# Kernel tuning notes

Measured on AMD Instinct MI355X. Metric: run time of the kernel, lower is better.

The kernel has to match this reference:

```python
import jax, jax.numpy as jnp
import numpy as np

BS, X_DIM, KEY_DIM, N_KEYS, TOPK = 16384, 4096, 512, 4096, 16


def setup_inputs() -> dict:
    key = jax.random.key(0)
    k_x, k_keys, k_w, k_b = jax.random.split(key, 4)
    bound = 1.0 / np.sqrt(X_DIM)  # torch Linear default init range
    return {
        "x": jax.random.normal(k_x, (BS, X_DIM), dtype=jnp.float32),
        "keys": jax.random.normal(k_keys, (N_KEYS, KEY_DIM), dtype=jnp.float32),
        "W": jax.random.uniform(k_w, (KEY_DIM, X_DIM), dtype=jnp.float32, minval=-bound, maxval=bound),
        "b": jax.random.uniform(k_b, (KEY_DIM,), dtype=jnp.float32, minval=-bound, maxval=bound),
        "topk": TOPK,
    }


def reference(x, keys, W, b, topk):
    # query = projection(x): [bs, key_dim]
    query = jnp.einsum("bx,kx->bk", x, W) + b
    # scores = query @ keys^T: [bs, n_keys]
    scores = jnp.einsum("bd,nd->bn", query, keys)
    real_topk = min(keys.shape[0], topk)
    topk_scores, topk_idx = jax.lax.top_k(scores, real_topk)  # [bs, k]
    bs = scores.shape[0]
    rows = jnp.arange(bs)[:, None]
    # scatter topk scores into a zero tensor, then softmax over the full row
    gates = jnp.zeros_like(scores).at[rows, topk_idx].set(topk_scores)
    gates = jax.nn.softmax(gates, axis=1)
    return (gates, scores)
```

## Files before the change

### kernel.cpp

```cpp
#include <hip/hip_runtime.h>
#include <stdint.h>

#define BS_T   16384
#define XDIM   4096
#define KDIM   512
#define NKEYS  4096
#define KTOP   16

typedef _Float16 half8  __attribute__((ext_vector_type(8)));
typedef _Float16 half4  __attribute__((ext_vector_type(4)));
typedef float    floatx4 __attribute__((ext_vector_type(4)));

__device__ static inline void gload_lds16(const void* g, void* l) {
  __builtin_amdgcn_global_load_lds(
      (const __attribute__((address_space(1))) uint32_t*)(uintptr_t)g,
      (__attribute__((address_space(3))) uint32_t*)(uint32_t)(uintptr_t)l,
      16, 0, 0);
}

#define SBAR() __builtin_amdgcn_sched_barrier(0)
#define FULL_BAR() do { __builtin_amdgcn_sched_barrier(0); \
                        __builtin_amdgcn_s_barrier(); \
                        __builtin_amdgcn_sched_barrier(0); } while (0)

__global__ __launch_bounds__(256) void cvt_f32_f16_v(const float* __restrict__ in,
                                                     _Float16* __restrict__ out, int n8) {
  int stride = gridDim.x * 256;
  for (int i = blockIdx.x * 256 + threadIdx.x; i < n8; i += stride) {
    float4 v0 = ((const float4*)in)[2 * i];
    float4 v1 = ((const float4*)in)[2 * i + 1];
    half8 h = { (_Float16)v0.x, (_Float16)v0.y, (_Float16)v0.z, (_Float16)v0.w,
                (_Float16)v1.x, (_Float16)v1.y, (_Float16)v1.z, (_Float16)v1.w };
    ((half8*)out)[i] = h;
  }
}

__global__ __launch_bounds__(512, 1)
void gemm1_pipe(const float* __restrict__ X, const _Float16* __restrict__ Wh,
                const float* __restrict__ bias, _Float16* __restrict__ Q) {
  __shared__ __align__(16) _Float16 ldsA[2][64 * 64];
  __shared__ __align__(16) _Float16 ldsB[2][512 * 64];

  const int tid  = threadIdx.x;
  const int lane = tid & 63;
  const int wid  = tid >> 6;
  const int rowBase = blockIdx.x * 64;
  const int rot  = (blockIdx.x * 29) & 63;
  const int wc  = wid * 64;
  const int l15 = lane & 15;
  const int q4  = lane >> 4;
  const int sub   = lane >> 3;
  const int gslot = (lane & 7) ^ sub;

  auto KT = [&](int t) { return ((t + rot) & 63) * 64; };

  const int r0 = tid >> 4,          s0 = tid & 15;
  const int r1 = (tid + 512) >> 4,  s1 = (tid + 512) & 15;
  const float* aSrc0 = X + (size_t)(rowBase + r0) * XDIM + s0 * 4;
  const float* aSrc1 = X + (size_t)(rowBase + r1) * XDIM + s1 * 4;
  const int aoff0 = r0 * 128 + (((s0 >> 1) * 16) ^ ((r0 & 7) << 4)) + (s0 & 1) * 8;
  const int aoff1 = r1 * 128 + (((s1 >> 1) * 16) ^ ((r1 & 7) << 4)) + (s1 & 1) * 8;

  const _Float16* const bSrc = Wh + (size_t)(wc + sub) * XDIM + gslot * 8;

  auto stageB = [&](int kt, int buf) {
    char* bd = (char*)&ldsB[buf][0] + wid * 8192;
    #pragma unroll
    for (int i = 0; i < 8; ++i)
      gload_lds16(bSrc + (size_t)i * 8 * XDIM + kt, bd + i * 1024);
  };
  auto writeA = [&](int buf, float4 v0, float4 v1) {
    half4 h0 = { (_Float16)v0.x, (_Float16)v0.y, (_Float16)v0.z, (_Float16)v0.w };
    half4 h1 = { (_Float16)v1.x, (_Float16)v1.y, (_Float16)v1.z, (_Float16)v1.w };
    *(half4*)((char*)&ldsA[buf][0] + aoff0) = h0;
    *(half4*)((char*)&ldsA[buf][0] + aoff1) = h1;
  };
  auto ld8 = [&](const char* base, int row, int s) {
    return *(const half8*)(base + row * 128 + ((s * 16) ^ ((row & 7) << 4)));
  };

  floatx4 acc[4][4];
  #pragma unroll
  for (int m = 0; m < 4; ++m)
    #pragma unroll
    for (int n = 0; n < 4; ++n)
      acc[m][n] = (floatx4)0.0f;

  float4 p0  = *(const float4*)(aSrc0 + KT(0));
  float4 p1  = *(const float4*)(aSrc1 + KT(0));
  float4 aw0 = *(const float4*)(aSrc0 + KT(1));
  float4 aw1 = *(const float4*)(aSrc1 + KT(1));
  stageB(KT(0), 0);
  stageB(KT(1), 1);
  writeA(0, p0, p1);
  asm volatile("s_waitcnt lgkmcnt(0)" ::: "memory");
  asm volatile("s_waitcnt vmcnt(8)" ::: "memory");
  FULL_BAR();

  #pragma unroll 2
  for (int t = 0; t < 64; ++t) {
    const int cu = t & 1;
    const char* bA = (const char*)&ldsA[cu][0];
    const char* bB = (const char*)&ldsB[cu][0];

    half8 a[4][2], b[4][2];
    #pragma unroll
    for (int m = 0; m < 4; ++m)
      #pragma unroll
      for (int kk = 0; kk < 2; ++kk)
        a[m][kk] = ld8(bA, m * 16 + l15, kk * 4 + q4);
    #pragma unroll
    for (int n = 0; n < 4; ++n)
      #pragma unroll
      for (int kk = 0; kk < 2; ++kk)
        b[n][kk] = ld8(bB, wc + n * 16 + l15, kk * 4 + q4);
    float4 nl0, nl1;
    if (t < 62) {
      nl0 = *(const float4*)(aSrc0 + KT(t + 2));
      nl1 = *(const float4*)(aSrc1 + KT(t + 2));
    }
    asm volatile("s_waitcnt lgkmcnt(0)" ::: "memory");
    __builtin_amdgcn_sched_barrier(0);
    if (t < 62) stageB(KT(t + 2), cu);
    __builtin_amdgcn_sched_barrier(0);

    __builtin_amdgcn_s_setprio(1);
    #pragma unroll
    for (int m = 0; m < 4; ++m)
      #pragma unroll
      for (int n = 0; n < 4; ++n)
        #pragma unroll
        for (int kk = 0; kk < 2; ++kk)
          acc[m][n] = __builtin_amdgcn_mfma_f32_16x16x32_f16(a[m][kk], b[n][kk], acc[m][n], 0, 0, 0);
    __builtin_amdgcn_s_setprio(0);

    if (t < 63) writeA(cu ^ 1, aw0, aw1);
    asm volatile("s_waitcnt lgkmcnt(0)" ::: "memory");
    __builtin_amdgcn_sched_barrier(0);
    if (t < 62)       asm volatile("s_waitcnt vmcnt(10)" ::: "memory");
    else if (t == 62) asm volatile("s_waitcnt vmcnt(0)"  ::: "memory");
    FULL_BAR();
    aw0 = nl0; aw1 = nl1;
  }

  #pragma unroll
  for (int m = 0; m < 4; ++m) {
    #pragma unroll
    for (int n = 0; n < 4; ++n) {
      int col = wc + n * 16 + l15;
      float bv = bias[col];
      #pragma unroll
      for (int r = 0; r < 4; ++r) {
        int row = rowBase + m * 16 + q4 * 4 + r;
        Q[(size_t)row * KDIM + col] = (_Float16)(acc[m][n][r] + bv);
      }
    }
  }
}

__global__ __launch_bounds__(512, 2)
void gemm2_pipe(const _Float16* __restrict__ Aq, const _Float16* __restrict__ Bk,
                float* __restrict__ outp) {
  __shared__ __align__(16) _Float16 ldsA[2][256 * 64];
  __shared__ __align__(16) _Float16 ldsB[2][256 * 64];

  const int tid  = threadIdx.x;
  const int lane = tid & 63;
  const int wid  = tid >> 6;
  const int bid  = blockIdx.x;
  const int nCol = NKEYS / 256;
  const int rowBase = (bid / nCol) * 256;
  const int colBase = (bid % nCol) * 256;
  const int wm = wid >> 2;
  const int wn = wid & 3;
  const int l15 = lane & 15;
  const int q4  = lane >> 4;
  const int sub   = lane >> 3;
  const int gslot = (lane & 7) ^ sub;

  const _Float16* aSrc = Aq + (size_t)rowBase * KDIM;
  const _Float16* bSrc = Bk + (size_t)colBase * KDIM;

  auto stageHalf = [&](const _Float16* src, char* ldsbase, int kt, int h) {
    #pragma unroll
    for (int j = 0; j < 2; ++j) {
      int g = h * 16 + wid * 2 + j;
      gload_lds16(src + (size_t)(g * 8 + sub) * KDIM + kt + gslot * 8,
                  ldsbase + g * 1024);
    }
  };
  auto ld8 = [&](const char* base, int row, int s) {
    return *(const half8*)(base + row * 128 + ((s * 16) ^ ((row & 7) << 4)));
  };

  floatx4 acc[8][4];
  #pragma unroll
  for (int m = 0; m < 8; ++m)
    #pragma unroll
    for (int n = 0; n < 4; ++n)
      acc[m][n] = (floatx4)0.0f;

  stageHalf(aSrc, (char*)ldsA[0], 0, 0);
  stageHalf(aSrc, (char*)ldsA[0], 0, 1);
  stageHalf(bSrc, (char*)ldsB[0], 0, 0);
  stageHalf(bSrc, (char*)ldsB[0], 0, 1);
  stageHalf(aSrc, (char*)ldsA[1], 64, 0);
  stageHalf(aSrc, (char*)ldsA[1], 64, 1);
  stageHalf(bSrc, (char*)ldsB[1], 64, 0);
  stageHalf(bSrc, (char*)ldsB[1], 64, 1);
  asm volatile("s_waitcnt vmcnt(8)" ::: "memory");
  FULL_BAR();

  for (int t = 0; t < 8; ++t) {
    const char* bA = (const char*)ldsA[t & 1];
    const char* bB = (const char*)ldsB[t & 1];
    char* sA = (char*)ldsA[t & 1];
    char* sB = (char*)ldsB[t & 1];
    const int ktn = (t + 2) * 64;
    const bool st = (t < 6);

    half8 a[4][2], b[4][2];

    #pragma unroll
    for (int m = 0; m < 4; ++m)
      #pragma unroll
      for (int kk = 0; kk < 2; ++kk)
        a[m][kk] = ld8(bA, wm * 128 + m * 16 + l15, kk * 4 + q4);
    #pragma unroll
    for (int n = 0; n < 4; ++n)
      #pragma unroll
      for (int kk = 0; kk < 2; ++kk)
        b[n][kk] = ld8(bB, wn * 64 + n * 16 + l15, kk * 4 + q4);
    FULL_BAR();
    asm volatile("s_waitcnt lgkmcnt(0)" ::: "memory");
    __builtin_amdgcn_sched_barrier(0);
    __builtin_amdgcn_s_setprio(1);
    #pragma unroll
    for (int m = 0; m < 4; ++m)
      #pragma unroll
      for (int n = 0; n < 2; ++n)
        #pragma unroll
        for (int kk = 0; kk < 2; ++kk)
          acc[m][n] = __builtin_amdgcn_mfma_f32_16x16x32_f16(a[m][kk], b[n][kk], acc[m][n], 0, 0, 0);
    __builtin_amdgcn_s_setprio(0);
    FULL_BAR();

    if (st) stageHalf(bSrc, sB, ktn, 0);
    __builtin_amdgcn_sched_barrier(0);
    __builtin_amdgcn_s_setprio(1);
    #pragma unroll
    for (int m = 0; m < 4; ++m)
      #pragma unroll
      for (int n = 2; n < 4; ++n)
        #pragma unroll
        for (int kk = 0; kk < 2; ++kk)
          acc[m][n] = __builtin_amdgcn_mfma_f32_16x16x32_f16(a[m][kk], b[n][kk], acc[m][n], 0, 0, 0);
    __builtin_amdgcn_s_setprio(0);
    FULL_BAR();

    #pragma unroll
    for (int m = 0; m < 4; ++m)
      #pragma unroll
      for (int kk = 0; kk < 2; ++kk)
        a[m][kk] = ld8(bA, wm * 128 + (m + 4) * 16 + l15, kk * 4 + q4);
    if (st) stageHalf(bSrc, sB, ktn, 1);
    FULL_BAR();
    asm volatile("s_waitcnt lgkmcnt(0)" ::: "memory");
    __builtin_amdgcn_sched_barrier(0);
    __builtin_amdgcn_s_setprio(1);
    #pragma unroll
    for (int m = 0; m < 4; ++m)
      #pragma unroll
      for (int n = 0; n < 2; ++n)
        #pragma unroll
        for (int kk = 0; kk < 2; ++kk)
          acc[m + 4][n] = __builtin_amdgcn_mfma_f32_16x16x32_f16(a[m][kk], b[n][kk], acc[m + 4][n], 0, 0, 0);
    __builtin_amdgcn_s_setprio(0);
    FULL_BAR();

    if (st) { stageHalf(aSrc, sA, ktn, 0); stageHalf(aSrc, sA, ktn, 1); }
    __builtin_amdgcn_sched_barrier(0);
    __builtin_amdgcn_s_setprio(1);
    #pragma unroll
    for (int m = 0; m < 4; ++m)
      #pragma unroll
      for (int n = 2; n < 4; ++n)
        #pragma unroll
        for (int kk = 0; kk < 2; ++kk)
          acc[m + 4][n] = __builtin_amdgcn_mfma_f32_16x16x32_f16(a[m][kk], b[n][kk], acc[m + 4][n], 0, 0, 0);
    __builtin_amdgcn_s_setprio(0);
    __builtin_amdgcn_sched_barrier(0);
    if (t < 6)      asm volatile("s_waitcnt vmcnt(8)" ::: "memory");
    else if (t == 6) asm volatile("s_waitcnt vmcnt(0)" ::: "memory");
    FULL_BAR();
  }

  #pragma unroll
  for (int m = 0; m < 8; ++m) {
    #pragma unroll
    for (int n = 0; n < 4; ++n) {
      int col = colBase + wn * 64 + n * 16 + l15;
      #pragma unroll
      for (int r = 0; r < 4; ++r) {
        int row = rowBase + wm * 128 + m * 16 + q4 * 4 + r;
        outp[(size_t)row * NKEYS + col] = acc[m][n][r];
      }
    }
  }
}

__global__ __launch_bounds__(256) void topk_gates_kernel(const float* __restrict__ scores,
                                                         float* __restrict__ gates) {
  __shared__ uint32_t hist[4096];
  __shared__ uint32_t sA[256];
  __shared__ uint32_t av[16], ai[16];
  __shared__ uint32_t sk[KTOP], si[KTOP];
  __shared__ uint32_t cntA, cntC;
  __shared__ int s_p; __shared__ uint32_t s_above;
  __shared__ float gk[KTOP]; __shared__ float s_gother;

  const int tid  = threadIdx.x;
  const int lane = tid & 63;
  const int w    = tid >> 6;
  const float* srow = scores + (size_t)blockIdx.x * NKEYS;

  uint4 z4 = {0, 0, 0, 0};
  #pragma unroll
  for (int i = 0; i < 4; ++i) ((uint4*)hist)[tid + 256 * i] = z4;
  if (tid == 0) { cntA = 0; cntC = 0; }

  uint32_t key[16];
  const int base = (w << 10) + (lane << 4);
  {
    const float4* p4 = (const float4*)(srow + base);
    #pragma unroll
    for (int i = 0; i < 4; ++i) {
      float4 t = p4[i];
      float tv[4] = { t.x, t.y, t.z, t.w };
      #pragma unroll
      for (int c = 0; c < 4; ++c) {
        uint32_t u = __float_as_uint(tv[c]);
        key[i * 4 + c] = u ^ (uint32_t)(((int32_t)u >> 31) | 0x80000000);
      }
    }
  }
  __syncthreads();

  #pragma unroll
  for (int j = 0; j < 16; ++j) atomicAdd(&hist[key[j] >> 20], 1u);
  __syncthreads();

  uint32_t h[16];
  #pragma unroll
  for (int i = 0; i < 16; ++i) h[i] = hist[tid * 16 + i];
  uint32_t sfx[17]; sfx[16] = 0;
  #pragma unroll
  for (int i = 15; i >= 0; --i) sfx[i] = sfx[i + 1] + h[i];
  sA[tid] = sfx[0];
  __syncthreads();
  uint32_t s = sfx[0];
  #pragma unroll
  for (int off = 1; off < 256; off <<= 1) {
    uint32_t add = (tid + off < 256) ? sA[tid + off] : 0;
    __syncthreads();
    s += add; sA[tid] = s;
    __syncthreads();
  }
  const uint32_t exclHi = s - sfx[0];

  #pragma unroll
  for (int i = 0; i < 16; ++i) {
    uint32_t cg = exclHi + sfx[i + 1];
    if (cg < KTOP && cg + h[i] >= KTOP) { s_p = tid * 16 + i; s_above = cg; }
  }
  __syncthreads();
  const uint32_t p = (uint32_t)s_p;
  const uint32_t above = s_above;
  const uint32_t need = KTOP - above;

  uint32_t* ck = hist;
  uint32_t* ci = hist + 2048;
  #pragma unroll
  for (int j = 0; j < 16; ++j) {
    uint32_t b = key[j] >> 20;
    if (b >= p) {
      uint32_t idx = (uint32_t)(base + j);
      if (b > p) { uint32_t pos = atomicAdd(&cntA, 1u); av[pos] = key[j]; ai[pos] = idx; }
      else       { uint32_t pos = atomicAdd(&cntC, 1u); if (pos < 2048u) { ck[pos] = key[j]; ci[pos] = idx; } }
    }
  }
  __syncthreads();

  const uint32_t nA = cntA;
  if (tid < nA) { sk[tid] = av[tid]; si[tid] = ai[tid]; }

  if (w == 0) {
    const uint32_t nC = min(cntC, 2048u);
    for (uint32_t k = 0; k < need; ++k) {
      uint32_t bk = 0, bi = 0xFFFFFFFFu, bp = 0;
      for (uint32_t c = lane; c < nC; c += 64) {
        uint32_t kk = ck[c], ii = ci[c];
        if (kk > bk || (kk == bk && ii < bi)) { bk = kk; bi = ii; bp = c; }
      }
      #pragma unroll
      for (int off = 32; off >= 1; off >>= 1) {
        uint32_t ok = __shfl_down(bk, off);
        uint32_t oi = __shfl_down(bi, off);
        uint32_t op = __shfl_down(bp, off);
        if (ok > bk || (ok == bk && oi < bi)) { bk = ok; bi = oi; bp = op; }
      }
      bp = __shfl(bp, 0);
      if (lane == 0) { ck[bp] = 0; sk[nA + k] = bk; si[nA + k] = bi; }
    }
  }
  __syncthreads();

  if (tid == 0) {
    float f[KTOP]; float mx = 0.f;
    #pragma unroll
    for (int k = 0; k < KTOP; ++k) {
      uint32_t kk = sk[k];
      float fv = (kk & 0x80000000u) ? __uint_as_float(kk ^ 0x80000000u)
                                    : __uint_as_float(~kk);
      f[k] = fv; mx = fmaxf(mx, fv);
    }
    float eo = __expf(-mx);
    float Z = (float)(NKEYS - KTOP) * eo;
    float e[KTOP];
    #pragma unroll
    for (int k = 0; k < KTOP; ++k) { e[k] = __expf(f[k] - mx); Z += e[k]; }
    float inv = 1.f / Z;
    #pragma unroll
    for (int k = 0; k < KTOP; ++k) gk[k] = e[k] * inv;
    s_gother = eo * inv;
  }
  __syncthreads();

  float go = s_gother;
  floatx4 g4 = { go, go, go, go };
  float* grow = gates + (size_t)blockIdx.x * NKEYS;
  #pragma unroll
  for (int j = 0; j < 4; ++j)
    __builtin_nontemporal_store(g4, (floatx4*)grow + j * 256 + tid);
  __syncthreads();
  if (tid < KTOP) grow[si[tid]] = gk[tid];
}

extern "C" void kernel_launch(void* const* d_in, const int* in_sizes, int n_in,
                              void* d_out, int out_size, void* d_ws, size_t ws_size,
                              hipStream_t stream) {
  const float* x    = (const float*)d_in[0];
  const float* keys = (const float*)d_in[1];
  const float* W    = (const float*)d_in[2];
  const float* bias = (const float*)d_in[3];
  (void)in_sizes; (void)n_in; (void)out_size; (void)ws_size;

  float* gates  = (float*)d_out;
  float* scores = (float*)d_out + (size_t)BS_T * NKEYS;

  _Float16* W_h = (_Float16*)d_ws;
  _Float16* k_h = W_h + (size_t)KDIM * XDIM;
  _Float16* q_h = k_h + (size_t)NKEYS * KDIM;

  cvt_f32_f16_v<<<dim3(1024), dim3(256), 0, stream>>>(W, W_h, KDIM * XDIM / 8);
  cvt_f32_f16_v<<<dim3(1024), dim3(256), 0, stream>>>(keys, k_h, NKEYS * KDIM / 8);

  gemm1_pipe<<<dim3(BS_T / 64), dim3(512), 0, stream>>>(x, W_h, bias, q_h);

  gemm2_pipe<<<dim3((BS_T / 256) * (NKEYS / 256)), dim3(512), 0, stream>>>(
      q_h, k_h, scores);

  topk_gates_kernel<<<dim3(BS_T), dim3(256), 0, stream>>>(scores, gates);
}
```

Baseline: 331.0 us.

## Shrink gemm2 tile to 128x128 with 4 waves and simplified single-phase pipeline

Reduces the scores GEMM block tile from 256x256 with 8 waves to 128x128 with 4 waves, with each wave computing a 64x64 sub-tile. The four interleaved MFMA phases and their separate staging steps are replaced by one stage call per k-step followed by a single MFMA block. This cuts LDS use and registers per block and launches four times as many blocks, trading lower operand reuse and higher global/L2 traffic for more occupancy and simpler scheduling.

```diff
diff --git a/kernel.cpp b/kernel.cpp
--- a/kernel.cpp
+++ b/kernel.cpp
@@ -158,21 +158,21 @@
   }
 }
 
-__global__ __launch_bounds__(512, 2)
+__global__ __launch_bounds__(256, 2)
 void gemm2_pipe(const _Float16* __restrict__ Aq, const _Float16* __restrict__ Bk,
                 float* __restrict__ outp) {
-  __shared__ __align__(16) _Float16 ldsA[2][256 * 64];
-  __shared__ __align__(16) _Float16 ldsB[2][256 * 64];
+  __shared__ __align__(16) _Float16 ldsA[2][128 * 64];
+  __shared__ __align__(16) _Float16 ldsB[2][128 * 64];
 
   const int tid  = threadIdx.x;
   const int lane = tid & 63;
   const int wid  = tid >> 6;
   const int bid  = blockIdx.x;
-  const int nCol = NKEYS / 256;
-  const int rowBase = (bid / nCol) * 256;
-  const int colBase = (bid % nCol) * 256;
-  const int wm = wid >> 2;
-  const int wn = wid & 3;
+  const int nCol = NKEYS / 128;
+  const int rowBase = (bid / nCol) * 128;
+  const int colBase = (bid % nCol) * 128;
+  const int wm = wid >> 1;
+  const int wn = wid & 1;
   const int l15 = lane & 15;
   const int q4  = lane >> 4;
   const int sub   = lane >> 3;
@@ -181,128 +181,78 @@
   const _Float16* aSrc = Aq + (size_t)rowBase * KDIM;
   const _Float16* bSrc = Bk + (size_t)colBase * KDIM;
 
-  auto stageHalf = [&](const _Float16* src, char* ldsbase, int kt, int h) {
-    #pragma unroll
-    for (int j = 0; j < 2; ++j) {
-      int g = h * 16 + wid * 2 + j;
-      gload_lds16(src + (size_t)(g * 8 + sub) * KDIM + kt + gslot * 8,
-                  ldsbase + g * 1024);
+  auto stage = [&](int kt, int buf) {
+    char* la = (char*)&ldsA[buf][0];
+    char* lb = (char*)&ldsB[buf][0];
+    #pragma unroll
+    for (int j = 0; j < 4; ++j) {
+      int g = wid * 4 + j;
+      gload_lds16(aSrc + (size_t)(g * 8 + sub) * KDIM + kt + gslot * 8, la + g * 1024);
+      gload_lds16(bSrc + (size_t)(g * 8 + sub) * KDIM + kt + gslot * 8, lb + g * 1024);
     }
   };
   auto ld8 = [&](const char* base, int row, int s) {
     return *(const half8*)(base + row * 128 + ((s * 16) ^ ((row & 7) << 4)));
   };
 
-  floatx4 acc[8][4];
-  #pragma unroll
-  for (int m = 0; m < 8; ++m)
+  floatx4 acc[4][4];
+  #pragma unroll
+  for (int m = 0; m < 4; ++m)
     #pragma unroll
     for (int n = 0; n < 4; ++n)
       acc[m][n] = (floatx4)0.0f;
 
-  stageHalf(aSrc, (char*)ldsA[0], 0, 0);
-  stageHalf(aSrc, (char*)ldsA[0], 0, 1);
-  stageHalf(bSrc, (char*)ldsB[0], 0, 0);
-  stageHalf(bSrc, (char*)ldsB[0], 0, 1);
-  stageHalf(aSrc, (char*)ldsA[1], 64, 0);
-  stageHalf(aSrc, (char*)ldsA[1], 64, 1);
-  stageHalf(bSrc, (char*)ldsB[1], 64, 0);
-  stageHalf(bSrc, (char*)ldsB[1], 64, 1);
+  stage(0, 0);
+  stage(64, 1);
   asm volatile("s_waitcnt vmcnt(8)" ::: "memory");
   FULL_BAR();
 
   for (int t = 0; t < 8; ++t) {
-    const char* bA = (const char*)ldsA[t & 1];
-    const char* bB = (const char*)ldsB[t & 1];
-    char* sA = (char*)ldsA[t & 1];
-    char* sB = (char*)ldsB[t & 1];
-    const int ktn = (t + 2) * 64;
-    const bool st = (t < 6);
+    const int cu = t & 1;
+    const char* bA = (const char*)&ldsA[cu][0];
+    const char* bB = (const char*)&ldsB[cu][0];
 
     half8 a[4][2], b[4][2];
-
     #pragma unroll
     for (int m = 0; m < 4; ++m)
       #pragma unroll
       for (int kk = 0; kk < 2; ++kk)
-        a[m][kk] = ld8(bA, wm * 128 + m * 16 + l15, kk * 4 + q4);
+        a[m][kk] = ld8(bA, wm * 64 + m * 16 + l15, kk * 4 + q4);
     #pragma unroll
     for (int n = 0; n < 4; ++n)
       #pragma unroll
       for (int kk = 0; kk < 2; ++kk)
         b[n][kk] = ld8(bB, wn * 64 + n * 16 + l15, kk * 4 + q4);
+    asm volatile("s_waitcnt lgkmcnt(0)" ::: "memory");
     FULL_BAR();
-    asm volatile("s_waitcnt lgkmcnt(0)" ::: "memory");
+
+    if (t < 6) stage((t + 2) * 64, cu);
     __builtin_amdgcn_sched_barrier(0);
+
     __builtin_amdgcn_s_setprio(1);
     #pragma unroll
     for (int m = 0; m < 4; ++m)
       #pragma unroll
-      for (int n = 0; n < 2; ++n)
+      for (int n = 0; n < 4; ++n)
         #pragma unroll
         for (int kk = 0; kk < 2; ++kk)
           acc[m][n] = __builtin_amdgcn_mfma_f32_16x16x32_f16(a[m][kk], b[n][kk], acc[m][n], 0, 0, 0);
     __builtin_amdgcn_s_setprio(0);
-    FULL_BAR();
-
-    if (st) stageHalf(bSrc, sB, ktn, 0);
     __builtin_amdgcn_sched_barrier(0);
-    __builtin_amdgcn_s_setprio(1);
-    #pragma unroll
-    for (int m = 0; m < 4; ++m)
-      #pragma unroll
-      for (int n = 2; n < 4; ++n)
-        #pragma unroll
-        for (int kk = 0; kk < 2; ++kk)
-          acc[m][n] = __builtin_amdgcn_mfma_f32_16x16x32_f16(a[m][kk], b[n][kk], acc[m][n], 0, 0, 0);
-    __builtin_amdgcn_s_setprio(0);
-    FULL_BAR();
-
-    #pragma unroll
-    for (int m = 0; m < 4; ++m)
-      #pragma unroll
-      for (int kk = 0; kk < 2; ++kk)
-        a[m][kk] = ld8(bA, wm * 128 + (m + 4) * 16 + l15, kk * 4 + q4);
-    if (st) stageHalf(bSrc, sB, ktn, 1);
-    FULL_BAR();
-    asm volatile("s_waitcnt lgkmcnt(0)" ::: "memory");
-    __builtin_amdgcn_sched_barrier(0);
-    __builtin_amdgcn_s_setprio(1);
-    #pragma unroll
-    for (int m = 0; m < 4; ++m)
-      #pragma unroll
-      for (int n = 0; n < 2; ++n)
-        #pragma unroll
-        for (int kk = 0; kk < 2; ++kk)
-          acc[m + 4][n] = __builtin_amdgcn_mfma_f32_16x16x32_f16(a[m][kk], b[n][kk], acc[m + 4][n], 0, 0, 0);
-    __builtin_amdgcn_s_setprio(0);
-    FULL_BAR();
-
-    if (st) { stageHalf(aSrc, sA, ktn, 0); stageHalf(aSrc, sA, ktn, 1); }
-    __builtin_amdgcn_sched_barrier(0);
-    __builtin_amdgcn_s_setprio(1);
-    #pragma unroll
-    for (int m = 0; m < 4; ++m)
-      #pragma unroll
-      for (int n = 2; n < 4; ++n)
-        #pragma unroll
-        for (int kk = 0; kk < 2; ++kk)
-          acc[m + 4][n] = __builtin_amdgcn_mfma_f32_16x16x32_f16(a[m][kk], b[n][kk], acc[m + 4][n], 0, 0, 0);
-    __builtin_amdgcn_s_setprio(0);
-    __builtin_amdgcn_sched_barrier(0);
+
     if (t < 6)      asm volatile("s_waitcnt vmcnt(8)" ::: "memory");
     else if (t == 6) asm volatile("s_waitcnt vmcnt(0)" ::: "memory");
     FULL_BAR();
   }
 
   #pragma unroll
-  for (int m = 0; m < 8; ++m) {
+  for (int m = 0; m < 4; ++m) {
     #pragma unroll
     for (int n = 0; n < 4; ++n) {
       int col = colBase + wn * 64 + n * 16 + l15;
       #pragma unroll
       for (int r = 0; r < 4; ++r) {
-        int row = rowBase + wm * 128 + m * 16 + q4 * 4 + r;
+        int row = rowBase + wm * 64 + m * 16 + q4 * 4 + r;
         outp[(size_t)row * NKEYS + col] = acc[m][n][r];
       }
     }
@@ -467,7 +417,7 @@
 
   gemm1_pipe<<<dim3(BS_T / 64), dim3(512), 0, stream>>>(x, W_h, bias, q_h);
 
-  gemm2_pipe<<<dim3((BS_T / 256) * (NKEYS / 256)), dim3(512), 0, stream>>>(
+  gemm2_pipe<<<dim3((BS_T / 128) * (NKEYS / 128)), dim3(256), 0, stream>>>(
       q_h, k_h, scores);
 
   topk_gates_kernel<<<dim3(BS_T), dim3(256), 0, stream>>>(scores, gates);
```

Result: no change. 325.7 us, median of 2 (-1.6%).
